# Kernel optimization log

Hardware: AMD Instinct MI355X
Metric: run time of the kernel (lower is better)

The kernel has to match this reference:

```python
import jax, jax.numpy as jnp
import numpy as np

B, N, F_IN, C_OUT = 128, 512, 2, 64
C_IN = F_IN + C_OUT           # 66, concat(input, state) feature dim
MLP_IN = (2 * 3 + 1) * C_IN   # order=2, support_len=3 -> 462


def _gcn(x, supports, W, b):
    """Diffusion conv: x [B,N,F]; for each support a, 2 diffusion orders."""
    outs = [x]
    for a in supports:
        x1 = jnp.einsum('bnf,nm->bmf', x, a)
        x2 = jnp.einsum('bnf,nm->bmf', x1, a)
        outs += [x1, x2]
    h = jnp.concatenate(outs, axis=2)  # [B, N, 7*F]
    return h @ W + b                   # Linear (dropout is eval-mode identity)


def setup_inputs() -> dict:
    key = jax.random.key(0)
    ks = jax.random.split(key, 12)
    return {
        'input': jax.random.normal(ks[0], (B, N, F_IN), dtype=jnp.float32),
        'state': jax.random.normal(ks[1], (B, N, C_OUT), dtype=jnp.float32),
        'A0':    jax.random.uniform(ks[2], (N, N), dtype=jnp.float32),
        'A1':    jax.random.uniform(ks[3], (N, N), dtype=jnp.float32),
        'nv1_1': jax.random.normal(ks[4], (N, 10), dtype=jnp.float32),
        'nv2_1': jax.random.normal(ks[5], (10, N), dtype=jnp.float32),
        'W1':    jax.random.normal(ks[6], (MLP_IN, 2 * C_OUT), dtype=jnp.float32) * 0.02,
        'b1':    jnp.zeros((2 * C_OUT,), dtype=jnp.float32),
        'nv1_2': jax.random.normal(ks[7], (N, 10), dtype=jnp.float32),
        'nv2_2': jax.random.normal(ks[8], (10, N), dtype=jnp.float32),
        'W2':    jax.random.normal(ks[9], (MLP_IN, C_OUT), dtype=jnp.float32) * 0.02,
        'b2':    jnp.zeros((C_OUT,), dtype=jnp.float32),
    }


def reference(input, state, A0, A1, nv1_1, nv2_1, W1, b1, nv1_2, nv2_2, W2, b2):
    c_out = state.shape[-1]
    # gcn_1: adaptive adjacency + diffusion conv, then sigmoid gating split into r,u
    adp1 = jax.nn.softmax(jax.nn.relu(nv1_1 @ nv2_1), axis=1)
    x = jnp.concatenate([input, state], axis=2)
    value = jax.nn.sigmoid(_gcn(x, [A0, A1, adp1], W1, b1))
    r, u = value[..., :c_out], value[..., c_out:]
    # gcn_2: candidate state
    adp2 = jax.nn.softmax(jax.nn.relu(nv1_2 @ nv2_2), axis=1)
    x2 = jnp.concatenate([input, r * state], axis=2)
    c = jnp.tanh(_gcn(x2, [A0, A1, adp2], W2, b2))
    return u * state + (1.0 - u) * c
```

## Files before the change

### kernel.cpp

```cpp
#include <hip/hip_runtime.h>
#include <math.h>

#define NN 512
#define BB 128
#define CIN 66
#define QQ (BB*CIN)
#define AN ((size_t)NN*NN)
#define HB 480
#define KTOT 480

typedef unsigned short ushort_t;
typedef __attribute__((ext_vector_type(8))) short short8;
typedef __attribute__((ext_vector_type(8))) unsigned short us8;
typedef __attribute__((ext_vector_type(4))) float f32x4;
typedef __attribute__((ext_vector_type(4))) unsigned short us4;

__device__ __forceinline__ size_t pidx(int b, int frow, int n) {
    return ((size_t)(b * 30 + (frow >> 4)) << 13) + ((size_t)(n >> 3) << 7)
         + ((frow & 15) << 3) + (n & 7);
}

__device__ __forceinline__ ushort_t f2bf(float f) {
    unsigned u = __float_as_uint(f);
    u += 0x7FFF + ((u >> 16) & 1);
    return (ushort_t)(u >> 16);
}
__device__ __forceinline__ float bf2f(ushort_t h) {
    return __uint_as_float(((unsigned)h) << 16);
}
__device__ __forceinline__ void split_bf(float f, ushort_t& hi, ushort_t& lo) {
    hi = f2bf(f);
    lo = f2bf(f - bf2f(hi));
}
__device__ __forceinline__ void gload_lds16(const void* g, void* l) {
    __builtin_amdgcn_global_load_lds(
        (const __attribute__((address_space(1))) unsigned*)g,
        (__attribute__((address_space(3))) unsigned*)l, 16, 0, 0);
}

__global__ __launch_bounds__(512) void adp_kernel(const float* __restrict__ nv1,
                                                  const float* __restrict__ nv2,
                                                  float* __restrict__ adp) {
    int n = blockIdx.x;
    int m = threadIdx.x;
    float z = 0.f;
#pragma unroll
    for (int k = 0; k < 10; k++) z = fmaf(nv1[n * 10 + k], nv2[k * NN + m], z);
    z = fmaxf(z, 0.f);

    __shared__ float sred[8];
    int wid  = threadIdx.x >> 6;
    int lane = threadIdx.x & 63;

    float v = z;
#pragma unroll
    for (int off = 32; off; off >>= 1) v = fmaxf(v, __shfl_down(v, off, 64));
    if (lane == 0) sred[wid] = v;
    __syncthreads();
    float zmax = sred[0];
#pragma unroll
    for (int i = 1; i < 8; i++) zmax = fmaxf(zmax, sred[i]);

    float e = __expf(z - zmax);
    __syncthreads();
    v = e;
#pragma unroll
    for (int off = 32; off; off >>= 1) v += __shfl_down(v, off, 64);
    if (lane == 0) sred[wid] = v;
    __syncthreads();
    float tot = 0.f;
#pragma unroll
    for (int i = 0; i < 8; i++) tot += sred[i];

    adp[n * NN + m] = e / tot;
}

__global__ __launch_bounds__(256) void asplit_kernel(const float* __restrict__ A0,
                                                     const float* __restrict__ A1,
                                                     const float* __restrict__ P1,
                                                     const float* __restrict__ P2,
                                                     ushort_t* __restrict__ Ahi,
                                                     ushort_t* __restrict__ Alo) {
    __shared__ float t[32][33];
    int s = blockIdx.z;
    const float* src = (s == 0) ? A0 : (s == 1) ? A1 : (s == 2) ? P1 : P2;
    int m0 = blockIdx.x * 32, k0 = blockIdx.y * 32;
    int tx = threadIdx.x & 31, ty = threadIdx.x >> 5;
#pragma unroll
    for (int r = 0; r < 32; r += 8)
        t[ty + r][tx] = src[(size_t)(k0 + ty + r) * NN + m0 + tx];
    __syncthreads();
#pragma unroll
    for (int r = 0; r < 32; r += 8) {
        int m = m0 + ty + r, k = k0 + tx;
        float v = t[tx][ty + r];
        ushort_t h, l; split_bf(v, h, l);
        int mt = m >> 4, l15 = m & 15;
        int kt = k >> 5, quad = (k >> 3) & 3, j = k & 7;
        size_t o = ((((size_t)s * 16 + kt) * 32 + mt) * 64 + quad * 16 + l15) * 8 + j;
        Ahi[o] = h; Alo[o] = l;
    }
}

template <int COUT>
__global__ __launch_bounds__(256) void wtprep_kernel(const float* __restrict__ W,
                                                     ushort_t* __restrict__ Wth,
                                                     ushort_t* __restrict__ Wtl) {
    int j = blockIdx.x;
    for (int k = threadIdx.x; k < KTOT; k += 256) {
        float v = (k < 462) ? W[(size_t)k * COUT + j] : 0.f;
        ushort_t h, l; split_bf(v, h, l);
        Wth[(size_t)j * KTOT + k] = h;
        Wtl[(size_t)j * KTOT + k] = l;
    }
}

__global__ __launch_bounds__(256) void buildx_kernel(const float* __restrict__ inp,
                                                     const float* __restrict__ st,
                                                     ushort_t* __restrict__ Xh,
                                                     ushort_t* __restrict__ Xl) {
    int gid = blockIdx.x * 256 + threadIdx.x;
    int ch  = gid & 63;
    int c   = (gid >> 6) % CIN;
    int b   = gid / (64 * CIN);
    int n0  = ch * 8;
    us8 h8, l8;
#pragma unroll
    for (int r = 0; r < 8; r++) {
        int n = n0 + r;
        float v = (c < 2) ? inp[((size_t)b * NN + n) * 2 + c]
                          : st[((size_t)b * NN + n) * 64 + (c - 2)];
        ushort_t h, l; split_bf(v, h, l);
        h8[r] = h; l8[r] = l;
    }
    size_t o = pidx(b, c, n0);
    *(us8*)&Xh[o] = h8;
    *(us8*)&Xl[o] = l8;
}

__global__ __launch_bounds__(512, 4) void diff_fused(const ushort_t* __restrict__ Aph,
                                                     const ushort_t* __restrict__ Apl,
                                                     ushort_t* Xh, ushort_t* Xl, int s2) {
    __shared__ ushort_t sX1h[32 * 520];
    __shared__ ushort_t sX1l[32 * 520];
    const int tid  = threadIdx.x;
    const int lane = tid & 63, w = tid >> 6;
    const int quad = lane >> 4, l15 = lane & 15;
    const int q0 = blockIdx.x * 32;
    const int sz = blockIdx.z;
    const int sup = (sz < 2) ? sz : s2;
    const size_t abase = (size_t)sup * 262144;
    const int mtg0 = w * 4;

    const ushort_t* xph[2];
    const ushort_t* xpl[2];
    int bq[2], cq[2];
#pragma unroll
    for (int qt = 0; qt < 2; qt++) {
        int q = q0 + qt * 16 + l15;
        int b = q / 66, c = q - 66 * b;
        bq[qt] = b; cq[qt] = c;
        size_t off = ((size_t)(b * 30 + (c >> 4)) << 13) + ((c & 15) << 3)
                   + (size_t)quad * 128;
        xph[qt] = Xh + off;
        xpl[qt] = Xl + off;
    }

#define DMFMA2(ACC, AH, AL, XH, XL)                                                                \
    {                                                                                              \
        _Pragma("unroll")                                                                          \
        for (int mt = 0; mt < 4; mt++) {                                                           \
            _Pragma("unroll")                                                                      \
            for (int qt = 0; qt < 2; qt++) {                                                       \
                ACC[mt][qt] = __builtin_amdgcn_mfma_f32_16x16x32_bf16(AH[mt], XH[qt], ACC[mt][qt], 0, 0, 0); \
                ACC[mt][qt] = __builtin_amdgcn_mfma_f32_16x16x32_bf16(AH[mt], XL[qt], ACC[mt][qt], 0, 0, 0); \
                ACC[mt][qt] = __builtin_amdgcn_mfma_f32_16x16x32_bf16(AL[mt], XH[qt], ACC[mt][qt], 0, 0, 0); \
                ACC[mt][qt] = __builtin_amdgcn_mfma_f32_16x16x32_bf16(AL[mt], XL[qt], ACC[mt][qt], 0, 0, 0); \
            }                                                                                      \
        }                                                                                          \
    }

    {
        f32x4 acc[4][2] = {};
        for (int kt = 0; kt < 16; kt++) {
            short8 ah[4], al[4], xh2[2], xl2[2];
#pragma unroll
            for (int t = 0; t < 4; t++) {
                size_t fo = abase + ((size_t)kt * 32 + mtg0 + t) * 512 + lane * 8;
                ah[t] = *(const short8*)&Aph[fo];
                al[t] = *(const short8*)&Apl[fo];
            }
#pragma unroll
            for (int qt = 0; qt < 2; qt++) {
                xh2[qt] = *(const short8*)&xph[qt][(size_t)kt * 512];
                xl2[qt] = *(const short8*)&xpl[qt][(size_t)kt * 512];
            }
            DMFMA2(acc, ah, al, xh2, xl2);
        }
        const int rowo = 66 + 132 * sz;
#pragma unroll
        for (int qt = 0; qt < 2; qt++) {
            int qloc = qt * 16 + l15;
            int frow = rowo + cq[qt];
#pragma unroll
            for (int mt = 0; mt < 4; mt++) {
                int n = w * 64 + mt * 16 + quad * 4;
                us4 h4, l4;
#pragma unroll
                for (int r = 0; r < 4; r++) {
                    ushort_t h, l; split_bf(acc[mt][qt][r], h, l);
                    h4[r] = h; l4[r] = l;
                }
                *(us4*)&sX1h[qloc * 520 + n] = h4;
                *(us4*)&sX1l[qloc * 520 + n] = l4;
                size_t o = pidx(bq[qt], frow, n);
                *(us4*)&Xh[o] = h4;
                *(us4*)&Xl[o] = l4;
            }
        }
    }
    __syncthreads();

    {
        f32x4 acc[4][2] = {};
        for (int kt = 0; kt < 16; kt++) {
            short8 ah[4], al[4], bh2[2], bl2[2];
#pragma unroll
            for (int t = 0; t < 4; t++) {
                size_t fo = abase + ((size_t)kt * 32 + mtg0 + t) * 512 + lane * 8;
                ah[t] = *(const short8*)&Aph[fo];
                al[t] = *(const short8*)&Apl[fo];
            }
#pragma unroll
            for (int qt = 0; qt < 2; qt++) {
                int idx = (qt * 16 + l15) * 520 + kt * 32 + quad * 8;
                bh2[qt] = *(const short8*)&sX1h[idx];
                bl2[qt] = *(const short8*)&sX1l[idx];
            }
            DMFMA2(acc, ah, al, bh2, bl2);
        }
        const int rowo = 132 + 132 * sz;
#pragma unroll
        for (int qt = 0; qt < 2; qt++) {
            int frow = rowo + cq[qt];
#pragma unroll
            for (int mt = 0; mt < 4; mt++) {
                int n = w * 64 + mt * 16 + quad * 4;
                us4 h4, l4;
#pragma unroll
                for (int r = 0; r < 4; r++) {
                    ushort_t h, l; split_bf(acc[mt][qt][r], h, l);
                    h4[r] = h; l4[r] = l;
                }
                size_t o = pidx(bq[qt], frow, n);
                *(us4*)&Xh[o] = h4;
                *(us4*)&Xl[o] = l4;
            }
        }
    }
#undef DMFMA2
}

template <int COUT, int LAYER, int BM>
__global__ __launch_bounds__(256) void proj_mfma(const ushort_t* XhC, const ushort_t* XlC,
                                                 const ushort_t* __restrict__ Wth,
                                                 const ushort_t* __restrict__ Wtl,
                                                 const float* __restrict__ bias,
                                                 const float* __restrict__ state,
                                                 float* U,
                                                 ushort_t* Xhw, ushort_t* Xlw,
                                                 float* __restrict__ out) {
    __shared__ ushort_t sAh[BM * 32];
    __shared__ ushort_t sAl[BM * 32];
    __shared__ ushort_t sBh[COUT * 32];
    __shared__ ushort_t sBl[COUT * 32];
    constexpr int PB = COUT / 64;
    const int tid  = threadIdx.x;
    const int lane = tid & 63, w = tid >> 6;
    const int quad = lane >> 4, l15 = lane & 15;
    const int b = blockIdx.y, n0 = blockIdx.x * BM;
    const int wn = (COUT == 128) ? (w & 1) : w;
    const int wj = (COUT == 128) ? (w >> 1) : 0;
    const int kp = tid & 15, n8 = tid >> 4;

    size_t boff[PB]; int lB[PB];
#pragma unroll
    for (int p = 0; p < PB; p++) {
        int cid = p * 256 + tid;
        lB[p]   = cid * 8;
        boff[p] = (size_t)(cid >> 2) * KTOT + (cid & 3) * 8;
    }

    f32x4 acc[4][4] = {};

    for (int k0 = 0; k0 < KTOT; k0 += 32) {
        __syncthreads();
#pragma unroll
        for (int pass = 0; pass < BM / 128; pass++) {
            int np0 = (n8 + pass * 16) * 8;
            int kk  = k0 + 2 * kp;
            size_t o = pidx(b, kk, n0 + np0);
            us8 h0 = *(const us8*)&XhC[o];
            us8 h1 = *(const us8*)&XhC[o + 8];
            us8 l0 = *(const us8*)&XlC[o];
            us8 l1 = *(const us8*)&XlC[o + 8];
            int g = kp >> 2, ko = (2 * kp) & 7;
#pragma unroll
            for (int j2 = 0; j2 < 8; j2++) {
                int n   = np0 + j2;
                int idx = n * 32 + ((g ^ ((n >> 1) & 3)) << 3) + ko;
                *(unsigned*)&sAh[idx] = (unsigned)h0[j2] | ((unsigned)h1[j2] << 16);
                *(unsigned*)&sAl[idx] = (unsigned)l0[j2] | ((unsigned)l1[j2] << 16);
            }
        }
#pragma unroll
        for (int p = 0; p < PB; p++) {
            gload_lds16(Wth + boff[p] + k0, sBh + lB[p]);
            gload_lds16(Wtl + boff[p] + k0, sBl + lB[p]);
        }
        __syncthreads();
        short8 ah[4], al[4], bh[4], bl[4];
#pragma unroll
        for (int t = 0; t < 4; t++) {
            int an  = wn * 64 + t * 16 + l15;
            int ago = (quad ^ ((an >> 1) & 3)) << 3;
            ah[t] = *(const short8*)&sAh[an * 32 + ago];
            al[t] = *(const short8*)&sAl[an * 32 + ago];
            int brow = wj * 64 + t * 16 + l15;
            bh[t] = *(const short8*)&sBh[brow * 32 + quad * 8];
            bl[t] = *(const short8*)&sBl[brow * 32 + quad * 8];
        }
#pragma unroll
        for (int nt = 0; nt < 4; nt++)
#pragma unroll
            for (int jt = 0; jt < 4; jt++) {
                acc[nt][jt] = __builtin_amdgcn_mfma_f32_16x16x32_bf16(ah[nt], bh[jt], acc[nt][jt], 0, 0, 0);
                acc[nt][jt] = __builtin_amdgcn_mfma_f32_16x16x32_bf16(ah[nt], bl[jt], acc[nt][jt], 0, 0, 0);
                acc[nt][jt] = __builtin_amdgcn_mfma_f32_16x16x32_bf16(al[nt], bh[jt], acc[nt][jt], 0, 0, 0);
                acc[nt][jt] = __builtin_amdgcn_mfma_f32_16x16x32_bf16(al[nt], bl[jt], acc[nt][jt], 0, 0, 0);
            }
    }

#pragma unroll
    for (int jt = 0; jt < 4; jt++) {
        int j = wj * 64 + jt * 16 + l15;
        float bj = bias[j];
#pragma unroll
        for (int nt = 0; nt < 4; nt++) {
            int nb = n0 + wn * 64 + nt * 16 + quad * 4;
            f32x4 z = acc[nt][jt];
#pragma unroll
            for (int r = 0; r < 4; r++) z[r] += bj;
            if (LAYER == 1) {
#pragma unroll
                for (int r = 0; r < 4; r++) z[r] = 1.f / (1.f + __expf(-z[r]));
                if (j < 64) {
                    us4 h4, l4;
#pragma unroll
                    for (int r = 0; r < 4; r++) {
                        float x2 = z[r] * state[((size_t)b * NN + nb + r) * 64 + j];
                        ushort_t h, l; split_bf(x2, h, l);
                        h4[r] = h; l4[r] = l;
                    }
                    size_t o = pidx(b, 2 + j, nb);
                    *(us4*)&Xhw[o] = h4;
                    *(us4*)&Xlw[o] = l4;
                } else {
                    *(f32x4*)&U[((size_t)b * 64 + j - 64) * NN + nb] = z;
                }
            } else {
                f32x4 u4 = *(const f32x4*)&U[((size_t)b * 64 + j) * NN + nb];
#pragma unroll
                for (int r = 0; r < 4; r++) {
                    float c = tanhf(z[r]);
                    float s = state[((size_t)b * NN + nb + r) * 64 + j];
                    out[((size_t)b * NN + nb + r) * 64 + j] = u4[r] * s + (1.f - u4[r]) * c;
                }
            }
        }
    }
}

extern "C" void kernel_launch(void* const* d_in, const int* in_sizes, int n_in,
                              void* d_out, int out_size, void* d_ws, size_t ws_size,
                              hipStream_t stream) {
    const float* input = (const float*)d_in[0];
    const float* state = (const float*)d_in[1];
    const float* A0    = (const float*)d_in[2];
    const float* A1    = (const float*)d_in[3];
    const float* nv1_1 = (const float*)d_in[4];
    const float* nv2_1 = (const float*)d_in[5];
    const float* W1    = (const float*)d_in[6];
    const float* b1    = (const float*)d_in[7];
    const float* nv1_2 = (const float*)d_in[8];
    const float* nv2_2 = (const float*)d_in[9];
    const float* W2    = (const float*)d_in[10];
    const float* b2    = (const float*)d_in[11];
    float* out = (float*)d_out;

    char* p = (char*)d_ws;
    auto alloc = [&](size_t bytes) { void* r = (void*)p; p += (bytes + 255) & ~(size_t)255; return r; };
    float*    ADP1 = (float*)alloc(AN * 4);
    float*    ADP2 = (float*)alloc(AN * 4);
    ushort_t* Ahi  = (ushort_t*)alloc(4 * AN * 2);
    ushort_t* Alo  = (ushort_t*)alloc(4 * AN * 2);
    ushort_t* Xh   = (ushort_t*)alloc((size_t)BB * HB * NN * 2);
    ushort_t* Xl   = (ushort_t*)alloc((size_t)BB * HB * NN * 2);
    ushort_t* Wt1h = (ushort_t*)alloc((size_t)128 * KTOT * 2);
    ushort_t* Wt1l = (ushort_t*)alloc((size_t)128 * KTOT * 2);
    ushort_t* Wt2h = (ushort_t*)alloc((size_t)64 * KTOT * 2);
    ushort_t* Wt2l = (ushort_t*)alloc((size_t)64 * KTOT * 2);
    float*    U    = (float*)alloc((size_t)BB * 64 * NN * 4);

    adp_kernel<<<NN, NN, 0, stream>>>(nv1_1, nv2_1, ADP1);
    adp_kernel<<<NN, NN, 0, stream>>>(nv1_2, nv2_2, ADP2);
    asplit_kernel<<<dim3(16, 16, 4), 256, 0, stream>>>(A0, A1, ADP1, ADP2, Ahi, Alo);
    wtprep_kernel<128><<<128, 256, 0, stream>>>(W1, Wt1h, Wt1l);
    wtprep_kernel<64><<<64, 256, 0, stream>>>(W2, Wt2h, Wt2l);
    buildx_kernel<<<BB * CIN * 64 / 256, 256, 0, stream>>>(input, state, Xh, Xl);

    dim3 gf(QQ / 32, 1, 3);
    diff_fused<<<gf, 512, 0, stream>>>(Ahi, Alo, Xh, Xl, 2);
    proj_mfma<128, 1, 128><<<dim3(NN / 128, BB), 256, 0, stream>>>(Xh, Xl, Wt1h, Wt1l, b1, state,
                                                                   U, Xh, Xl, nullptr);
    diff_fused<<<gf, 512, 0, stream>>>(Ahi, Alo, Xh, Xl, 3);
    proj_mfma<64, 2, 256><<<dim3(NN / 256, BB), 256, 0, stream>>>(Xh, Xl, Wt2h, Wt2l, b2, state,
                                                                  U, nullptr, nullptr, out);
}
```

Measured before the change: 417.7 us.

## Widen diffusion tile to 64 columns and read first-hop output from global

Each diffusion block now covers 64 batch-feature columns instead of 32, so every loaded adjacency fragment feeds twice as many MFMAs. The LDS staging of the first-hop result is removed; after the block barrier, the second hop reads that result back from global memory, where the same block just wrote it. This cuts adjacency load traffic and frees LDS. The costs are a larger accumulator array (more register pressure), a dropped occupancy hint in the launch bounds, and half as many blocks, which can leave the 396-block grid unevenly spread across CUs. The second hop also now relies on its own global writes being visible after __syncthreads.

```diff
diff --git a/kernel.cpp b/kernel.cpp
--- a/kernel.cpp
+++ b/kernel.cpp
@@ -138,40 +138,32 @@
     *(us8*)&Xl[o] = l8;
 }
 
-__global__ __launch_bounds__(512, 4) void diff_fused(const ushort_t* __restrict__ Aph,
-                                                     const ushort_t* __restrict__ Apl,
-                                                     ushort_t* Xh, ushort_t* Xl, int s2) {
-    __shared__ ushort_t sX1h[32 * 520];
-    __shared__ ushort_t sX1l[32 * 520];
+__global__ __launch_bounds__(512) void diff_fused(const ushort_t* __restrict__ Aph,
+                                                  const ushort_t* __restrict__ Apl,
+                                                  ushort_t* Xh, ushort_t* Xl, int s2) {
     const int tid  = threadIdx.x;
     const int lane = tid & 63, w = tid >> 6;
     const int quad = lane >> 4, l15 = lane & 15;
-    const int q0 = blockIdx.x * 32;
+    const int q0 = blockIdx.x * 64;
     const int sz = blockIdx.z;
     const int sup = (sz < 2) ? sz : s2;
     const size_t abase = (size_t)sup * 262144;
     const int mtg0 = w * 4;
 
-    const ushort_t* xph[2];
-    const ushort_t* xpl[2];
-    int bq[2], cq[2];
-#pragma unroll
-    for (int qt = 0; qt < 2; qt++) {
+    int bq[4], cq[4];
+#pragma unroll
+    for (int qt = 0; qt < 4; qt++) {
         int q = q0 + qt * 16 + l15;
-        int b = q / 66, c = q - 66 * b;
-        bq[qt] = b; cq[qt] = c;
-        size_t off = ((size_t)(b * 30 + (c >> 4)) << 13) + ((c & 15) << 3)
-                   + (size_t)quad * 128;
-        xph[qt] = Xh + off;
-        xpl[qt] = Xl + off;
-    }
-
-#define DMFMA2(ACC, AH, AL, XH, XL)                                                                \
+        bq[qt] = q / 66;
+        cq[qt] = q - 66 * bq[qt];
+    }
+
+#define DMFMA4(ACC, AH, AL, XH, XL)                                                                \
     {                                                                                              \
         _Pragma("unroll")                                                                          \
         for (int mt = 0; mt < 4; mt++) {                                                           \
             _Pragma("unroll")                                                                      \
-            for (int qt = 0; qt < 2; qt++) {                                                       \
+            for (int qt = 0; qt < 4; qt++) {                                                       \
                 ACC[mt][qt] = __builtin_amdgcn_mfma_f32_16x16x32_bf16(AH[mt], XH[qt], ACC[mt][qt], 0, 0, 0); \
                 ACC[mt][qt] = __builtin_amdgcn_mfma_f32_16x16x32_bf16(AH[mt], XL[qt], ACC[mt][qt], 0, 0, 0); \
                 ACC[mt][qt] = __builtin_amdgcn_mfma_f32_16x16x32_bf16(AL[mt], XH[qt], ACC[mt][qt], 0, 0, 0); \
@@ -181,9 +173,19 @@
     }
 
     {
-        f32x4 acc[4][2] = {};
+        const ushort_t* xph[4];
+        const ushort_t* xpl[4];
+#pragma unroll
+        for (int qt = 0; qt < 4; qt++) {
+            int c = cq[qt];
+            size_t off = ((size_t)(bq[qt] * 30 + (c >> 4)) << 13) + ((c & 15) << 3)
+                       + (size_t)quad * 128;
+            xph[qt] = Xh + off;
+            xpl[qt] = Xl + off;
+        }
+        f32x4 acc[4][4] = {};
         for (int kt = 0; kt < 16; kt++) {
-            short8 ah[4], al[4], xh2[2], xl2[2];
+            short8 ah[4], al[4], xh4[4], xl4[4];
 #pragma unroll
             for (int t = 0; t < 4; t++) {
                 size_t fo = abase + ((size_t)kt * 32 + mtg0 + t) * 512 + lane * 8;
@@ -191,57 +193,15 @@
                 al[t] = *(const short8*)&Apl[fo];
             }
 #pragma unroll
-            for (int qt = 0; qt < 2; qt++) {
-                xh2[qt] = *(const short8*)&xph[qt][(size_t)kt * 512];
-                xl2[qt] = *(const short8*)&xpl[qt][(size_t)kt * 512];
-            }
-            DMFMA2(acc, ah, al, xh2, xl2);
+            for (int qt = 0; qt < 4; qt++) {
+                xh4[qt] = *(const short8*)&xph[qt][(size_t)kt * 512];
+                xl4[qt] = *(const short8*)&xpl[qt][(size_t)kt * 512];
+            }
+            DMFMA4(acc, ah, al, xh4, xl4);
         }
         const int rowo = 66 + 132 * sz;
 #pragma unroll
-        for (int qt = 0; qt < 2; qt++) {
-            int qloc = qt * 16 + l15;
-            int frow = rowo + cq[qt];
-#pragma unroll
-            for (int mt = 0; mt < 4; mt++) {
-                int n = w * 64 + mt * 16 + quad * 4;
-                us4 h4, l4;
-#pragma unroll
-                for (int r = 0; r < 4; r++) {
-                    ushort_t h, l; split_bf(acc[mt][qt][r], h, l);
-                    h4[r] = h; l4[r] = l;
-                }
-                *(us4*)&sX1h[qloc * 520 + n] = h4;
-                *(us4*)&sX1l[qloc * 520 + n] = l4;
-                size_t o = pidx(bq[qt], frow, n);
-                *(us4*)&Xh[o] = h4;
-                *(us4*)&Xl[o] = l4;
-            }
-        }
-    }
-    __syncthreads();
-
-    {
-        f32x4 acc[4][2] = {};
-        for (int kt = 0; kt < 16; kt++) {
-            short8 ah[4], al[4], bh2[2], bl2[2];
-#pragma unroll
-            for (int t = 0; t < 4; t++) {
-                size_t fo = abase + ((size_t)kt * 32 + mtg0 + t) * 512 + lane * 8;
-                ah[t] = *(const short8*)&Aph[fo];
-                al[t] = *(const short8*)&Apl[fo];
-            }
-#pragma unroll
-            for (int qt = 0; qt < 2; qt++) {
-                int idx = (qt * 16 + l15) * 520 + kt * 32 + quad * 8;
-                bh2[qt] = *(const short8*)&sX1h[idx];
-                bl2[qt] = *(const short8*)&sX1l[idx];
-            }
-            DMFMA2(acc, ah, al, bh2, bl2);
-        }
-        const int rowo = 132 + 132 * sz;
-#pragma unroll
-        for (int qt = 0; qt < 2; qt++) {
+        for (int qt = 0; qt < 4; qt++) {
             int frow = rowo + cq[qt];
 #pragma unroll
             for (int mt = 0; mt < 4; mt++) {
@@ -258,7 +218,56 @@
             }
         }
     }
-#undef DMFMA2
+    __syncthreads();
+
+    {
+        const int rowi = 66 + 132 * sz;
+        const ushort_t* xph[4];
+        const ushort_t* xpl[4];
+#pragma unroll
+        for (int qt = 0; qt < 4; qt++) {
+            int frow = rowi + cq[qt];
+            size_t off = ((size_t)(bq[qt] * 30 + (frow >> 4)) << 13) + ((frow & 15) << 3)
+                       + (size_t)quad * 128;
+            xph[qt] = Xh + off;
+            xpl[qt] = Xl + off;
+        }
+        f32x4 acc[4][4] = {};
+        for (int kt = 0; kt < 16; kt++) {
+            short8 ah[4], al[4], xh4[4], xl4[4];
+#pragma unroll
+            for (int t = 0; t < 4; t++) {
+                size_t fo = abase + ((size_t)kt * 32 + mtg0 + t) * 512 + lane * 8;
+                ah[t] = *(const short8*)&Aph[fo];
+                al[t] = *(const short8*)&Apl[fo];
+            }
+#pragma unroll
+            for (int qt = 0; qt < 4; qt++) {
+                xh4[qt] = *(const short8*)&xph[qt][(size_t)kt * 512];
+                xl4[qt] = *(const short8*)&xpl[qt][(size_t)kt * 512];
+            }
+            DMFMA4(acc, ah, al, xh4, xl4);
+        }
+        const int rowo = 132 + 132 * sz;
+#pragma unroll
+        for (int qt = 0; qt < 4; qt++) {
+            int frow = rowo + cq[qt];
+#pragma unroll
+            for (int mt = 0; mt < 4; mt++) {
+                int n = w * 64 + mt * 16 + quad * 4;
+                us4 h4, l4;
+#pragma unroll
+                for (int r = 0; r < 4; r++) {
+                    ushort_t h, l; split_bf(acc[mt][qt][r], h, l);
+                    h4[r] = h; l4[r] = l;
+                }
+                size_t o = pidx(bq[qt], frow, n);
+                *(us4*)&Xh[o] = h4;
+                *(us4*)&Xl[o] = l4;
+            }
+        }
+    }
+#undef DMFMA4
 }
 
 template <int COUT, int LAYER, int BM>
@@ -419,7 +428,7 @@
     wtprep_kernel<64><<<64, 256, 0, stream>>>(W2, Wt2h, Wt2l);
     buildx_kernel<<<BB * CIN * 64 / 256, 256, 0, stream>>>(input, state, Xh, Xl);
 
-    dim3 gf(QQ / 32, 1, 3);
+    dim3 gf(QQ / 64, 1, 3);
     diff_fused<<<gf, 512, 0, stream>>>(Ahi, Alo, Xh, Xl, 2);
     proj_mfma<128, 1, 128><<<dim3(NN / 128, BB), 256, 0, stream>>>(Xh, Xl, Wt1h, Wt1l, b1, state,
                                                                    U, Xh, Xl, nullptr);
```

New measurement: 417.9 us. No clear change (+0.1%).
